# Optimization experiments

Hardware: AMD Instinct MI355X
Metric: run time of the kernel (lower is better)

The kernel has to match this reference:

```python
import jax, jax.numpy as jnp
import numpy as np

N = 8192      # sequence length (rows of query/key/value)
D = 768       # model dim (Conv1d in_channels)
DFF = 2048    # FFN hidden dim (Conv1d out_channels)


def setup_inputs() -> dict:
    key = jax.random.key(0)
    ks = jax.random.split(key, 7)
    query = jax.random.normal(ks[0], (N, D), dtype=jnp.float32)
    k = jax.random.normal(ks[1], (N, D), dtype=jnp.float32)
    value = jax.random.normal(ks[2], (N, D), dtype=jnp.float32)
    # Conv1d(kernel_size=1) == dense layer: weight [out,in], bias [out]
    W1 = jax.random.normal(ks[3], (DFF, D), dtype=jnp.float32) * 0.02
    b1 = jax.random.normal(ks[4], (DFF,), dtype=jnp.float32) * 0.02
    W2 = jax.random.normal(ks[5], (D, DFF), dtype=jnp.float32) * 0.02
    b2 = jax.random.normal(ks[6], (D,), dtype=jnp.float32) * 0.02
    return {"query": query, "key": k, "value": value,
            "W1": W1, "b1": b1, "W2": W2, "b2": b2}


def reference(query, key, value, W1, b1, W2, b2):
    # manual attention: no 1/sqrt(d) scaling in the original module
    scores = jnp.matmul(query, key.T)              # [N, N]
    attn = jax.nn.softmax(scores, axis=-1)         # [N, N]
    context = jnp.matmul(attn, value)              # [N, D]
    # conv1x1 -> ReLU -> conv1x1 (2-layer MLP)
    h = jax.nn.relu(jnp.matmul(context, W1.T) + b1)  # [N, DFF]
    out = jnp.matmul(h, W2.T) + b2                   # [N, D]
    return out
```

## Files before the change

### kernel.cpp

```cpp
#include <hip/hip_runtime.h>
#include <cstdint>
#include <cstddef>

#define DEV __device__ __forceinline__

typedef _Float16 f16;
typedef __attribute__((ext_vector_type(8))) _Float16 f16x8;
typedef __attribute__((ext_vector_type(4))) float f32x4;

DEV unsigned short f2h(float f) {
  f16 h = (f16)f;
  return __builtin_bit_cast(unsigned short, h);
}

DEV void async_ld16(const void* g, void* l) {
  __builtin_amdgcn_global_load_lds(
      (__attribute__((address_space(1))) unsigned int*)(uintptr_t)g,
      (__attribute__((address_space(3))) unsigned int*)(uint32_t)(uintptr_t)l,
      16, 0, 0);
}

#define MFMA16(d, a, b_) (d) = __builtin_amdgcn_mfma_f32_16x16x32_f16((a), (b_), (d), 0, 0, 0)

template <int EPI, bool RELU, bool HASBIAS, bool ALPHA, bool XCD>
__global__ __launch_bounds__(512, 2) void gemm256(
    const unsigned short* __restrict__ A, const unsigned short* __restrict__ B,
    void* __restrict__ Cp, const float* __restrict__ bias,
    const unsigned short* __restrict__ alp, int Mtot,
    int K, int lda, int ldb, int ldc, int nt, int mt, int sl) {
  extern __shared__ char smem[];
  const int NT = K >> 6;

  int mb, nb, zb;
  {
    const int b = blockIdx.x;
    if (XCD) {
      const int xcd = b & 7, q = b >> 3;
      nb = q % nt;
      const int rest = q / nt;
      zb = rest % sl;
      mb = xcd * (mt >> 3) + rest / sl;
    } else {
      nb = b % nt;
      const int t = b / nt;
      mb = t % mt;
      zb = t / mt;
    }
  }
  const int bm = mb << 8, bn = nb << 8;
  const unsigned koff = (unsigned)zb * (unsigned)K;

  const int tid = threadIdx.x;
  const int wave = tid >> 6, lane = tid & 63;
  const int wr = wave >> 2, wc = wave & 3;
  const int mr = lane & 15, quad = lane >> 4;

  const int slot = tid & 7, rr = tid >> 3;
  const int ce = (slot ^ (rr & 7)) << 3;

  f32x4 acc[8][4] = {};
  f16x8 av0[4][2], av1[4][2], bv0[2][2], bv1[2][2];
  const f16* alb = (const f16*)(smem + 131072);

  if (ALPHA) {
    const int ntl = K >> 7;
    const unsigned short* g0 = alp + (size_t)(zb * ntl) * Mtot + bm;
    uint4* s = (uint4*)(smem + 131072);
    const int nu4 = (ntl << 5);
    for (int idx = tid; idx < nu4; idx += 512) {
      const int tt = idx >> 5;
      const int ru = (idx & 31) << 3;
      s[idx] = *(const uint4*)(g0 + (size_t)tt * Mtot + ru);
    }
  }

  auto stA = [&](int h, int Ts) {
    const int t_ = Ts >= NT ? Ts - NT : Ts;
    const unsigned kk = koff + (unsigned)(t_ << 6);
    char* l = smem + ((Ts & 1) << 16) + h * 16384 + wave * 1024;
#pragma unroll
    for (int p = 0; p < 2; ++p) {
      const unsigned off = (unsigned)(bm + p * 128 + h * 64 + rr) * (unsigned)lda + kk + ce;
      async_ld16(A + off, l + p * 8192);
    }
  };
  auto stB = [&](int h, int Ts) {
    const int t_ = Ts >= NT ? Ts - NT : Ts;
    const unsigned kk = koff + (unsigned)(t_ << 6);
    char* l = smem + ((Ts & 1) << 16) + 32768 + h * 16384 + wave * 1024;
#pragma unroll
    for (int p = 0; p < 2; ++p) {
      const unsigned off =
          (unsigned)(bn + p * 128 + (rr >> 5) * 64 + h * 32 + (rr & 31)) * (unsigned)ldb + kk + ce;
      async_ld16(B + off, l + p * 8192);
    }
  };
  auto rdA = [&](int bufc, int i, int ks) {
    const int r = wr * 64 + (i & 3) * 16 + mr;
    return *(const f16x8*)(smem + bufc + (i >> 2) * 16384 + r * 128 +
                           ((((ks << 2) | quad) ^ (mr & 7)) << 4));
  };
  auto rdB = [&](int bufc, int j, int ks) {
    const int r = wc * 32 + (j & 1) * 16 + mr;
    return *(const f16x8*)(smem + bufc + 32768 + (j >> 1) * 16384 + r * 128 +
                           ((((ks << 2) | quad) ^ (mr & 7)) << 4));
  };

  stA(0, 0); stB(0, 0); stA(1, 0); stB(1, 0);
  stA(0, 1); stB(0, 1); stA(1, 1);
  if (ALPHA) asm volatile("s_waitcnt lgkmcnt(0)" ::: "memory");
  asm volatile("s_waitcnt vmcnt(6)" ::: "memory");
  __builtin_amdgcn_s_barrier();

  for (int T = 0; T < NT; ++T) {
    const int bufc = (T & 1) << 16;
    f16 a0_[4], a1_[4];
#pragma unroll
    for (int i = 0; i < 4; ++i) { av0[i][0] = rdA(bufc, i, 0); av0[i][1] = rdA(bufc, i, 1); }
    if (ALPHA) {
#pragma unroll
      for (int i = 0; i < 4; ++i) a0_[i] = alb[(T >> 1) * 256 + wr * 128 + i * 16 + mr];
    }
    stB(1, T + 1);
    __builtin_amdgcn_s_barrier();
    asm volatile("s_waitcnt lgkmcnt(0)" ::: "memory");
    __builtin_amdgcn_sched_barrier(0);
    if (ALPHA) {
#pragma unroll
      for (int i = 0; i < 4; ++i) { av0[i][0] = av0[i][0] * a0_[i]; av0[i][1] = av0[i][1] * a0_[i]; }
    }
    if (T) {
      __builtin_amdgcn_s_setprio(1);
#pragma unroll
      for (int i = 0; i < 4; ++i)
#pragma unroll
        for (int j = 0; j < 2; ++j) {
          MFMA16(acc[4 + i][2 + j], av1[i][0], bv1[j][0]);
          MFMA16(acc[4 + i][2 + j], av1[i][1], bv1[j][1]);
        }
      __builtin_amdgcn_s_setprio(0);
    }
    __builtin_amdgcn_s_barrier();
#pragma unroll
    for (int j = 0; j < 2; ++j) { bv0[j][0] = rdB(bufc, j, 0); bv0[j][1] = rdB(bufc, j, 1); }
    stA(0, T + 2);
    __builtin_amdgcn_s_barrier();
    asm volatile("s_waitcnt lgkmcnt(0)" ::: "memory");
    __builtin_amdgcn_sched_barrier(0);
    __builtin_amdgcn_s_setprio(1);
#pragma unroll
    for (int i = 0; i < 4; ++i)
#pragma unroll
      for (int j = 0; j < 2; ++j) {
        MFMA16(acc[i][j], av0[i][0], bv0[j][0]);
        MFMA16(acc[i][j], av0[i][1], bv0[j][1]);
      }
    __builtin_amdgcn_s_setprio(0);
    __builtin_amdgcn_s_barrier();
#pragma unroll
    for (int i = 0; i < 4; ++i) { av1[i][0] = rdA(bufc, 4 + i, 0); av1[i][1] = rdA(bufc, 4 + i, 1); }
    if (ALPHA) {
#pragma unroll
      for (int i = 0; i < 4; ++i) a1_[i] = alb[(T >> 1) * 256 + wr * 128 + 64 + i * 16 + mr];
    }
    stB(0, T + 2);
    __builtin_amdgcn_s_barrier();
    asm volatile("s_waitcnt lgkmcnt(0)" ::: "memory");
    __builtin_amdgcn_sched_barrier(0);
    if (ALPHA) {
#pragma unroll
      for (int i = 0; i < 4; ++i) { av1[i][0] = av1[i][0] * a1_[i]; av1[i][1] = av1[i][1] * a1_[i]; }
    }
    __builtin_amdgcn_s_setprio(1);
#pragma unroll
    for (int i = 0; i < 4; ++i)
#pragma unroll
      for (int j = 0; j < 2; ++j) {
        MFMA16(acc[4 + i][j], av1[i][0], bv0[j][0]);
        MFMA16(acc[4 + i][j], av1[i][1], bv0[j][1]);
      }
    __builtin_amdgcn_s_setprio(0);
    __builtin_amdgcn_s_barrier();
#pragma unroll
    for (int j = 0; j < 2; ++j) { bv1[j][0] = rdB(bufc, 2 + j, 0); bv1[j][1] = rdB(bufc, 2 + j, 1); }
    stA(1, T + 2);
    __builtin_amdgcn_s_barrier();
    asm volatile("s_waitcnt lgkmcnt(0)" ::: "memory");
    __builtin_amdgcn_sched_barrier(0);
    __builtin_amdgcn_s_setprio(1);
#pragma unroll
    for (int i = 0; i < 4; ++i)
#pragma unroll
      for (int j = 0; j < 2; ++j) {
        MFMA16(acc[i][2 + j], av0[i][0], bv1[j][0]);
        MFMA16(acc[i][2 + j], av0[i][1], bv1[j][1]);
      }
    __builtin_amdgcn_s_setprio(0);
    asm volatile("s_waitcnt vmcnt(6)" ::: "memory");
    __builtin_amdgcn_s_barrier();
  }
  __builtin_amdgcn_s_setprio(1);
#pragma unroll
  for (int i = 0; i < 4; ++i)
#pragma unroll
    for (int j = 0; j < 2; ++j) {
      MFMA16(acc[4 + i][2 + j], av1[i][0], bv1[j][0]);
      MFMA16(acc[4 + i][2 + j], av1[i][1], bv1[j][1]);
    }
  __builtin_amdgcn_s_setprio(0);
  asm volatile("s_waitcnt vmcnt(0)" ::: "memory");
  __builtin_amdgcn_s_barrier();

#pragma unroll
  for (int i = 0; i < 8; ++i) {
#pragma unroll
    for (int j = 0; j < 4; ++j) {
      const int col = bn + wc * 64 + j * 16 + mr;
      float bb = 0.f;
      if (HASBIAS) bb = bias[col];
#pragma unroll
      for (int r = 0; r < 4; ++r) {
        const int row = bm + wr * 128 + i * 16 + quad * 4 + r;
        float v = acc[i][j][r];
        if (HASBIAS) v += bb;
        if (RELU) v = fmaxf(v, 0.f);
        if (EPI == 2)
          atomicAdd(&((float*)Cp)[(size_t)row * ldc + col], v);
        else
          ((unsigned short*)Cp)[(size_t)row * ldc + col] = f2h(v);
      }
    }
  }
}

__global__ __launch_bounds__(512, 2) void qk256(
    const unsigned short* __restrict__ A, const unsigned short* __restrict__ B,
    unsigned short* __restrict__ P, float* __restrict__ stm,
    float* __restrict__ stl, int M, int K, int lda, int ldb, int ldc) {
  extern __shared__ char smem[];
  const int NT = K >> 6;

  const int b = blockIdx.x;
  const int xcd = b & 7, c = b >> 3;
  const int mb = c & 31, nb = (xcd << 2) | (c >> 5);
  const int bm = mb << 8, bn = nb << 8;

  const int tid = threadIdx.x;
  const int wave = tid >> 6, lane = tid & 63;
  const int wr = wave >> 2, wc = wave & 3;
  const int mr = lane & 15, quad = lane >> 4;

  const int slot = tid & 7, rr = tid >> 3;
  const int ce = (slot ^ (rr & 7)) << 3;

  f32x4 acc[8][4] = {};
  f16x8 av0[4][2], av1[4][2], bv0[2][2], bv1[2][2];

  auto stA = [&](int h, int Ts) {
    const int t = Ts >= NT ? Ts - NT : Ts;
    const int kk = t << 6;
    char* l = smem + ((Ts & 1) << 16) + h * 16384 + wave * 1024;
#pragma unroll
    for (int p = 0; p < 2; ++p) {
      const unsigned off = (unsigned)(bm + p * 128 + h * 64 + rr) * (unsigned)lda + kk + ce;
      async_ld16(A + off, l + p * 8192);
    }
  };
  auto stB = [&](int h, int Ts) {
    const int t = Ts >= NT ? Ts - NT : Ts;
    const int kk = t << 6;
    char* l = smem + ((Ts & 1) << 16) + 32768 + h * 16384 + wave * 1024;
#pragma unroll
    for (int p = 0; p < 2; ++p) {
      const unsigned off =
          (unsigned)(bn + p * 128 + (rr >> 5) * 64 + h * 32 + (rr & 31)) * (unsigned)ldb + kk + ce;
      async_ld16(B + off, l + p * 8192);
    }
  };
  auto rdA = [&](int bufc, int i, int ks) {
    const int r = wr * 64 + (i & 3) * 16 + mr;
    return *(const f16x8*)(smem + bufc + (i >> 2) * 16384 + r * 128 +
                           ((((ks << 2) | quad) ^ (mr & 7)) << 4));
  };
  auto rdB = [&](int bufc, int j, int ks) {
    const int r = wc * 32 + (j & 1) * 16 + mr;
    return *(const f16x8*)(smem + bufc + 32768 + (j >> 1) * 16384 + r * 128 +
                           ((((ks << 2) | quad) ^ (mr & 7)) << 4));
  };

  stA(0, 0); stB(0, 0); stA(1, 0); stB(1, 0);
  stA(0, 1); stB(0, 1); stA(1, 1);
  asm volatile("s_waitcnt vmcnt(6)" ::: "memory");
  __builtin_amdgcn_s_barrier();

  for (int T = 0; T < NT; ++T) {
    const int bufc = (T & 1) << 16;
#pragma unroll
    for (int i = 0; i < 4; ++i) { av0[i][0] = rdA(bufc, i, 0); av0[i][1] = rdA(bufc, i, 1); }
    stB(1, T + 1);
    __builtin_amdgcn_s_barrier();
    asm volatile("s_waitcnt lgkmcnt(0)" ::: "memory");
    __builtin_amdgcn_sched_barrier(0);
    if (T) {
      __builtin_amdgcn_s_setprio(1);
#pragma unroll
      for (int i = 0; i < 4; ++i)
#pragma unroll
        for (int j = 0; j < 2; ++j) {
          MFMA16(acc[4 + i][2 + j], av1[i][0], bv1[j][0]);
          MFMA16(acc[4 + i][2 + j], av1[i][1], bv1[j][1]);
        }
      __builtin_amdgcn_s_setprio(0);
    }
    __builtin_amdgcn_s_barrier();
#pragma unroll
    for (int j = 0; j < 2; ++j) { bv0[j][0] = rdB(bufc, j, 0); bv0[j][1] = rdB(bufc, j, 1); }
    stA(0, T + 2);
    __builtin_amdgcn_s_barrier();
    asm volatile("s_waitcnt lgkmcnt(0)" ::: "memory");
    __builtin_amdgcn_sched_barrier(0);
    __builtin_amdgcn_s_setprio(1);
#pragma unroll
    for (int i = 0; i < 4; ++i)
#pragma unroll
      for (int j = 0; j < 2; ++j) {
        MFMA16(acc[i][j], av0[i][0], bv0[j][0]);
        MFMA16(acc[i][j], av0[i][1], bv0[j][1]);
      }
    __builtin_amdgcn_s_setprio(0);
    __builtin_amdgcn_s_barrier();
#pragma unroll
    for (int i = 0; i < 4; ++i) { av1[i][0] = rdA(bufc, 4 + i, 0); av1[i][1] = rdA(bufc, 4 + i, 1); }
    stB(0, T + 2);
    __builtin_amdgcn_s_barrier();
    asm volatile("s_waitcnt lgkmcnt(0)" ::: "memory");
    __builtin_amdgcn_sched_barrier(0);
    __builtin_amdgcn_s_setprio(1);
#pragma unroll
    for (int i = 0; i < 4; ++i)
#pragma unroll
      for (int j = 0; j < 2; ++j) {
        MFMA16(acc[4 + i][j], av1[i][0], bv0[j][0]);
        MFMA16(acc[4 + i][j], av1[i][1], bv0[j][1]);
      }
    __builtin_amdgcn_s_setprio(0);
    __builtin_amdgcn_s_barrier();
#pragma unroll
    for (int j = 0; j < 2; ++j) { bv1[j][0] = rdB(bufc, 2 + j, 0); bv1[j][1] = rdB(bufc, 2 + j, 1); }
    stA(1, T + 2);
    __builtin_amdgcn_s_barrier();
    asm volatile("s_waitcnt lgkmcnt(0)" ::: "memory");
    __builtin_amdgcn_sched_barrier(0);
    __builtin_amdgcn_s_setprio(1);
#pragma unroll
    for (int i = 0; i < 4; ++i)
#pragma unroll
      for (int j = 0; j < 2; ++j) {
        MFMA16(acc[i][2 + j], av0[i][0], bv1[j][0]);
        MFMA16(acc[i][2 + j], av0[i][1], bv1[j][1]);
      }
    __builtin_amdgcn_s_setprio(0);
    asm volatile("s_waitcnt vmcnt(6)" ::: "memory");
    __builtin_amdgcn_s_barrier();
  }
  __builtin_amdgcn_s_setprio(1);
#pragma unroll
  for (int i = 0; i < 4; ++i)
#pragma unroll
    for (int j = 0; j < 2; ++j) {
      MFMA16(acc[4 + i][2 + j], av1[i][0], bv1[j][0]);
      MFMA16(acc[4 + i][2 + j], av1[i][1], bv1[j][1]);
    }
  __builtin_amdgcn_s_setprio(0);
  asm volatile("s_waitcnt vmcnt(0)" ::: "memory");
  __builtin_amdgcn_s_barrier();

  float* sred = (float*)smem;
  float* ssum = (float*)(smem + 4096);
  const int hc = wc >> 1;
  float Mh[8][4];

#pragma unroll
  for (int i = 0; i < 8; ++i)
#pragma unroll
    for (int r = 0; r < 4; ++r) {
      float m = acc[i][0][r];
#pragma unroll
      for (int j = 1; j < 4; ++j) m = fmaxf(m, acc[i][j][r]);
      m = fmaxf(m, __shfl_xor(m, 1));
      m = fmaxf(m, __shfl_xor(m, 2));
      m = fmaxf(m, __shfl_xor(m, 4));
      m = fmaxf(m, __shfl_xor(m, 8));
      if (mr == 0) sred[(wr * 128 + i * 16 + quad * 4 + r) * 4 + wc] = m;
    }
  __syncthreads();
#pragma unroll
  for (int i = 0; i < 8; ++i)
#pragma unroll
    for (int r = 0; r < 4; ++r) {
      const int row_l = wr * 128 + i * 16 + quad * 4 + r;
      Mh[i][r] = fmaxf(sred[row_l * 4 + 2 * hc], sred[row_l * 4 + 2 * hc + 1]);
    }
#pragma unroll
  for (int i = 0; i < 8; ++i)
#pragma unroll
    for (int r = 0; r < 4; ++r) {
      const int row_l = wr * 128 + i * 16 + quad * 4 + r;
      float l = 0.f;
#pragma unroll
      for (int j = 0; j < 4; ++j) {
        const float e = __expf(acc[i][j][r] - Mh[i][r]);
        P[(size_t)(bm + row_l) * ldc + (bn + wc * 64 + j * 16 + mr)] = f2h(e);
        l += e;
      }
      l += __shfl_xor(l, 1);
      l += __shfl_xor(l, 2);
      l += __shfl_xor(l, 4);
      l += __shfl_xor(l, 8);
      if (mr == 0) ssum[row_l * 4 + wc] = l;
    }
  __syncthreads();
  if ((wc & 1) == 0 && mr == 0) {
#pragma unroll
    for (int i = 0; i < 8; ++i)
#pragma unroll
      for (int r = 0; r < 4; ++r) {
        const int row_l = wr * 128 + i * 16 + quad * 4 + r;
        const int tile = nb * 2 + hc;
        stm[(size_t)tile * M + bm + row_l] = Mh[i][r];
        stl[(size_t)tile * M + bm + row_l] =
            ssum[row_l * 4 + 2 * hc] + ssum[row_l * 4 + 2 * hc + 1];
      }
  }
}

__global__ __launch_bounds__(256) void combine_alpha(
    const float* __restrict__ stm, const float* __restrict__ stl,
    unsigned short* __restrict__ alp, int ntile, int Mtot) {
  const int row = blockIdx.x * 4 + (threadIdx.x >> 6);
  const int t = threadIdx.x & 63;
  float m = (t < ntile) ? stm[(size_t)t * Mtot + row] : -1e30f;
  float M = m;
#pragma unroll
  for (int o = 1; o < 64; o <<= 1) M = fmaxf(M, __shfl_xor(M, o));
  float l = (t < ntile) ? stl[(size_t)t * Mtot + row] : 0.f;
  float c = l * __expf(m - M);
#pragma unroll
  for (int o = 1; o < 64; o <<= 1) c += __shfl_xor(c, o);
  if (t < ntile) alp[(size_t)t * Mtot + row] = f2h(__expf(m - M) / c);
}

__global__ __launch_bounds__(256) void cvt_f16(const float* __restrict__ in,
                                               unsigned short* __restrict__ out, int n) {
  int i = blockIdx.x * 256 + threadIdx.x;
  if (i < n) out[i] = f2h(in[i]);
}

__global__ __launch_bounds__(256) void bias_fill(float* __restrict__ out,
                                                 const float* __restrict__ b, int d) {
  int i = blockIdx.x * 256 + threadIdx.x;
  out[i] = b[i % d];
}

__global__ __launch_bounds__(256) void vt_kernel(const float* __restrict__ V,
                                                 unsigned short* __restrict__ vT) {
  __shared__ float t[32][33];
  const int bx = blockIdx.x, by = blockIdx.y;
  const int x = threadIdx.x, y = threadIdx.y;
#pragma unroll
  for (int r = 0; r < 4; ++r)
    t[y + r * 8][x] = V[(size_t)(by * 32 + y + r * 8) * 768 + bx * 32 + x];
  __syncthreads();
#pragma unroll
  for (int r = 0; r < 4; ++r)
    vT[(size_t)(bx * 32 + y + r * 8) * 8192 + by * 32 + x] = f2h(t[x][y + r * 8]);
}

extern "C" void kernel_launch(void* const* d_in, const int* in_sizes, int n_in,
                              void* d_out, int out_size, void* d_ws, size_t ws_size,
                              hipStream_t stream) {
  const int N = 8192, D = 768, DFF = 2048;
  const float* Q  = (const float*)d_in[0];
  const float* Km = (const float*)d_in[1];
  const float* V  = (const float*)d_in[2];
  const float* W1 = (const float*)d_in[3];
  const float* b1 = (const float*)d_in[4];
  const float* W2 = (const float*)d_in[5];
  const float* b2 = (const float*)d_in[6];

  char* w = (char*)d_ws;
  size_t off = 0;
  auto take = [&](size_t bytes) { void* p = w + off; off += bytes; return p; };
  unsigned short* qh   = (unsigned short*)take((size_t)N * D * 2);
  unsigned short* kh   = (unsigned short*)take((size_t)N * D * 2);
  unsigned short* vT   = (unsigned short*)take((size_t)N * D * 2);
  unsigned short* ctx16= (unsigned short*)take((size_t)N * D * 2);
  float*          ctx32= (float*)take((size_t)N * D * 4);
  unsigned short* hb   = (unsigned short*)take((size_t)N * DFF * 2);
  unsigned short* w1h  = (unsigned short*)take((size_t)DFF * D * 2);
  unsigned short* w2h  = (unsigned short*)take((size_t)D * DFF * 2);
  float*          stm  = (float*)take((size_t)64 * N * 4);
  float*          stl  = (float*)take((size_t)64 * N * 4);
  unsigned short* alp  = (unsigned short*)take((size_t)64 * N * 2);
  unsigned short* Pp   = (unsigned short*)take((size_t)N * N * 2);
  (void)ws_size;

  cvt_f16<<<(N * D) / 256, 256, 0, stream>>>(Q, qh, N * D);
  cvt_f16<<<(N * D) / 256, 256, 0, stream>>>(Km, kh, N * D);
  vt_kernel<<<dim3(D / 32, N / 32), dim3(32, 8), 0, stream>>>(V, vT);
  cvt_f16<<<(DFF * D) / 256, 256, 0, stream>>>(W1, w1h, DFF * D);
  cvt_f16<<<(D * DFF) / 256, 256, 0, stream>>>(W2, w2h, D * DFF);
  hipMemsetAsync(ctx32, 0, (size_t)N * D * 4, stream);
  bias_fill<<<(N * D) / 256, 256, 0, stream>>>((float*)d_out, b2, D);

  {
    hipFuncSetAttribute((const void*)qk256,
                        hipFuncAttributeMaxDynamicSharedMemorySize, 131072);
    qk256<<<(N / 256) * (N / 256), 512, 131072, stream>>>(
        qh, kh, Pp, stm, stl, N, D, D, D, N);
  }
  combine_alpha<<<N / 4, 256, 0, stream>>>(stm, stl, alp, 64, N);

  {
    const int nt = D / 256, mt = N / 256, sl = 2;
    const int smem_sz = 131072 + ((N / sl) >> 7) * 256 * 2;
    hipFuncSetAttribute((const void*)gemm256<2, false, false, true, true>,
                        hipFuncAttributeMaxDynamicSharedMemorySize, smem_sz);
    gemm256<2, false, false, true, true><<<nt * mt * sl, 512, smem_sz, stream>>>(
        Pp, vT, ctx32, nullptr, alp, N,
        N / sl, N, N, D, nt, mt, sl);
  }
  cvt_f16<<<(N * D) / 256, 256, 0, stream>>>(ctx32, ctx16, N * D);

  {
    const int nt = DFF / 256, mt = N / 256;
    hipFuncSetAttribute((const void*)gemm256<0, true, true, false, true>,
                        hipFuncAttributeMaxDynamicSharedMemorySize, 131072);
    gemm256<0, true, true, false, true><<<nt * mt, 512, 131072, stream>>>(
        ctx16, w1h, hb, b1, nullptr, N,
        D, D, D, DFF, nt, mt, 1);
  }
  {
    const int nt = D / 256, mt = N / 256, sl = 2;
    hipFuncSetAttribute((const void*)gemm256<2, false, false, false, true>,
                        hipFuncAttributeMaxDynamicSharedMemorySize, 131072);
    gemm256<2, false, false, false, true><<<nt * mt * sl, 512, 131072, stream>>>(
        hb, w2h, (float*)d_out, nullptr, nullptr, N,
        DFF / sl, DFF, DFF, D, nt, mt, sl);
  }
}
```

Baseline: 576.0 us.

## Add 256x192 tile variant for D-output GEMMs to improve CU fill

Templates the GEMM on output tile width BN and adds a 192-column variant with its own B-tile LDS layout, load mapping and fragment reads. The attention-times-V and second FFN GEMMs (output width 768) now use 256x192 tiles, so 4 N-tiles instead of 3 and more workgroups to fill the GPU. The trade-offs are lower arithmetic intensity per tile, an uneven LDS load split for the B operand, and more atomic split-K traffic in total.

```diff
diff --git a/kernel.cpp b/kernel.cpp
--- a/kernel.cpp
+++ b/kernel.cpp
@@ -22,13 +22,16 @@
 
 #define MFMA16(d, a, b_) (d) = __builtin_amdgcn_mfma_f32_16x16x32_f16((a), (b_), (d), 0, 0, 0)
 
-template <int EPI, bool RELU, bool HASBIAS, bool ALPHA, bool XCD>
+template <int BN, int EPI, bool RELU, bool HASBIAS, bool ALPHA, bool XCD>
 __global__ __launch_bounds__(512, 2) void gemm256(
     const unsigned short* __restrict__ A, const unsigned short* __restrict__ B,
     void* __restrict__ Cp, const float* __restrict__ bias,
     const unsigned short* __restrict__ alp, int Mtot,
     int K, int lda, int ldb, int ldc, int nt, int mt, int sl) {
   extern __shared__ char smem[];
+  constexpr int FN = BN / 64;
+  constexpr int WCW = BN / 4;
+  constexpr int BUFSZ = 32768 + BN * 128;
   const int NT = K >> 6;
 
   int mb, nb, zb;
@@ -47,7 +50,7 @@
       zb = t / mt;
     }
   }
-  const int bm = mb << 8, bn = nb << 8;
+  const int bm = mb << 8, bn = nb * BN;
   const unsigned koff = (unsigned)zb * (unsigned)K;
 
   const int tid = threadIdx.x;
@@ -58,14 +61,14 @@
   const int slot = tid & 7, rr = tid >> 3;
   const int ce = (slot ^ (rr & 7)) << 3;
 
-  f32x4 acc[8][4] = {};
-  f16x8 av0[4][2], av1[4][2], bv0[2][2], bv1[2][2];
-  const f16* alb = (const f16*)(smem + 131072);
+  f32x4 acc[8][FN] = {};
+  f16x8 av0[4][2], av1[4][2], bv0[2][2], bv1[FN - 2][2];
+  const f16* alb = (const f16*)(smem + 2 * BUFSZ);
 
   if (ALPHA) {
     const int ntl = K >> 7;
     const unsigned short* g0 = alp + (size_t)(zb * ntl) * Mtot + bm;
-    uint4* s = (uint4*)(smem + 131072);
+    uint4* s = (uint4*)(smem + 2 * BUFSZ);
     const int nu4 = (ntl << 5);
     for (int idx = tid; idx < nu4; idx += 512) {
       const int tt = idx >> 5;
@@ -77,7 +80,7 @@
   auto stA = [&](int h, int Ts) {
     const int t_ = Ts >= NT ? Ts - NT : Ts;
     const unsigned kk = koff + (unsigned)(t_ << 6);
-    char* l = smem + ((Ts & 1) << 16) + h * 16384 + wave * 1024;
+    char* l = smem + (Ts & 1) * BUFSZ + h * 16384 + wave * 1024;
 #pragma unroll
     for (int p = 0; p < 2; ++p) {
       const unsigned off = (unsigned)(bm + p * 128 + h * 64 + rr) * (unsigned)lda + kk + ce;
@@ -87,12 +90,22 @@
   auto stB = [&](int h, int Ts) {
     const int t_ = Ts >= NT ? Ts - NT : Ts;
     const unsigned kk = koff + (unsigned)(t_ << 6);
-    char* l = smem + ((Ts & 1) << 16) + 32768 + h * 16384 + wave * 1024;
-#pragma unroll
-    for (int p = 0; p < 2; ++p) {
-      const unsigned off =
-          (unsigned)(bn + p * 128 + (rr >> 5) * 64 + h * 32 + (rr & 31)) * (unsigned)ldb + kk + ce;
-      async_ld16(B + off, l + p * 8192);
+    char* l = smem + (Ts & 1) * BUFSZ + 32768 + h * 16384 + wave * 1024;
+    if (BN == 256) {
+#pragma unroll
+      for (int p = 0; p < 2; ++p) {
+        const int g = bn + p * 128 + (rr >> 5) * 64 + h * 32 + (rr & 31);
+        async_ld16(B + ((unsigned)g * (unsigned)ldb + kk + ce), l + p * 8192);
+      }
+    } else if (h == 0) {
+#pragma unroll
+      for (int p = 0; p < 2; ++p) {
+        const int g = bn + (p * 2 + (rr >> 5)) * 48 + (rr & 31);
+        async_ld16(B + ((unsigned)g * (unsigned)ldb + kk + ce), l + p * 8192);
+      }
+    } else {
+      const int g = bn + (rr >> 4) * 48 + 32 + (rr & 15);
+      async_ld16(B + ((unsigned)g * (unsigned)ldb + kk + ce), l);
     }
   };
   auto rdA = [&](int bufc, int i, int ks) {
@@ -100,9 +113,14 @@
     return *(const f16x8*)(smem + bufc + (i >> 2) * 16384 + r * 128 +
                            ((((ks << 2) | quad) ^ (mr & 7)) << 4));
   };
-  auto rdB = [&](int bufc, int j, int ks) {
-    const int r = wc * 32 + (j & 1) * 16 + mr;
-    return *(const f16x8*)(smem + bufc + 32768 + (j >> 1) * 16384 + r * 128 +
+  auto rdB0 = [&](int bufc, int j, int ks) {
+    const int rb = wc * 32 + j * 16 + mr;
+    return *(const f16x8*)(smem + bufc + 32768 + rb * 128 +
+                           ((((ks << 2) | quad) ^ (mr & 7)) << 4));
+  };
+  auto rdB1 = [&](int bufc, int j, int ks) {
+    const int rb = (BN == 256) ? (wc * 32 + (j - 2) * 16 + mr) : (wc * 16 + mr);
+    return *(const f16x8*)(smem + bufc + 32768 + 16384 + rb * 128 +
                            ((((ks << 2) | quad) ^ (mr & 7)) << 4));
   };
 
@@ -113,7 +131,7 @@
   __builtin_amdgcn_s_barrier();
 
   for (int T = 0; T < NT; ++T) {
-    const int bufc = (T & 1) << 16;
+    const int bufc = (T & 1) * BUFSZ;
     f16 a0_[4], a1_[4];
 #pragma unroll
     for (int i = 0; i < 4; ++i) { av0[i][0] = rdA(bufc, i, 0); av0[i][1] = rdA(bufc, i, 1); }
@@ -134,7 +152,7 @@
 #pragma unroll
       for (int i = 0; i < 4; ++i)
 #pragma unroll
-        for (int j = 0; j < 2; ++j) {
+        for (int j = 0; j < FN - 2; ++j) {
           MFMA16(acc[4 + i][2 + j], av1[i][0], bv1[j][0]);
           MFMA16(acc[4 + i][2 + j], av1[i][1], bv1[j][1]);
         }
@@ -142,7 +160,7 @@
     }
     __builtin_amdgcn_s_barrier();
 #pragma unroll
-    for (int j = 0; j < 2; ++j) { bv0[j][0] = rdB(bufc, j, 0); bv0[j][1] = rdB(bufc, j, 1); }
+    for (int j = 0; j < 2; ++j) { bv0[j][0] = rdB0(bufc, j, 0); bv0[j][1] = rdB0(bufc, j, 1); }
     stA(0, T + 2);
     __builtin_amdgcn_s_barrier();
     asm volatile("s_waitcnt lgkmcnt(0)" ::: "memory");
@@ -182,7 +200,7 @@
     __builtin_amdgcn_s_setprio(0);
     __builtin_amdgcn_s_barrier();
 #pragma unroll
-    for (int j = 0; j < 2; ++j) { bv1[j][0] = rdB(bufc, 2 + j, 0); bv1[j][1] = rdB(bufc, 2 + j, 1); }
+    for (int j = 0; j < FN - 2; ++j) { bv1[j][0] = rdB1(bufc, 2 + j, 0); bv1[j][1] = rdB1(bufc, 2 + j, 1); }
     stA(1, T + 2);
     __builtin_amdgcn_s_barrier();
     asm volatile("s_waitcnt lgkmcnt(0)" ::: "memory");
@@ -191,7 +209,7 @@
 #pragma unroll
     for (int i = 0; i < 4; ++i)
 #pragma unroll
-      for (int j = 0; j < 2; ++j) {
+      for (int j = 0; j < FN - 2; ++j) {
         MFMA16(acc[i][2 + j], av0[i][0], bv1[j][0]);
         MFMA16(acc[i][2 + j], av0[i][1], bv1[j][1]);
       }
@@ -203,7 +221,7 @@
 #pragma unroll
   for (int i = 0; i < 4; ++i)
 #pragma unroll
-    for (int j = 0; j < 2; ++j) {
+    for (int j = 0; j < FN - 2; ++j) {
       MFMA16(acc[4 + i][2 + j], av1[i][0], bv1[j][0]);
       MFMA16(acc[4 + i][2 + j], av1[i][1], bv1[j][1]);
     }
@@ -214,8 +232,8 @@
 #pragma unroll
   for (int i = 0; i < 8; ++i) {
 #pragma unroll
-    for (int j = 0; j < 4; ++j) {
-      const int col = bn + wc * 64 + j * 16 + mr;
+    for (int j = 0; j < FN; ++j) {
+      const int col = bn + wc * WCW + j * 16 + mr;
       float bb = 0.f;
       if (HASBIAS) bb = bias[col];
 #pragma unroll
@@ -522,11 +540,12 @@
   combine_alpha<<<N / 4, 256, 0, stream>>>(stm, stl, alp, 64, N);
 
   {
-    const int nt = D / 256, mt = N / 256, sl = 2;
-    const int smem_sz = 131072 + ((N / sl) >> 7) * 256 * 2;
-    hipFuncSetAttribute((const void*)gemm256<2, false, false, true, true>,
+    const int nt = D / 192, mt = N / 256, sl = 2;
+    constexpr int BUFSZ = 32768 + 192 * 128;
+    const int smem_sz = 2 * BUFSZ + ((N / 2) >> 7) * 256 * 2;
+    hipFuncSetAttribute((const void*)gemm256<192, 2, false, false, true, true>,
                         hipFuncAttributeMaxDynamicSharedMemorySize, smem_sz);
-    gemm256<2, false, false, true, true><<<nt * mt * sl, 512, smem_sz, stream>>>(
+    gemm256<192, 2, false, false, true, true><<<nt * mt * sl, 512, smem_sz, stream>>>(
         Pp, vT, ctx32, nullptr, alp, N,
         N / sl, N, N, D, nt, mt, sl);
   }
@@ -534,17 +553,18 @@
 
   {
     const int nt = DFF / 256, mt = N / 256;
-    hipFuncSetAttribute((const void*)gemm256<0, true, true, false, true>,
+    hipFuncSetAttribute((const void*)gemm256<256, 0, true, true, false, true>,
                         hipFuncAttributeMaxDynamicSharedMemorySize, 131072);
-    gemm256<0, true, true, false, true><<<nt * mt, 512, 131072, stream>>>(
+    gemm256<256, 0, true, true, false, true><<<nt * mt, 512, 131072, stream>>>(
         ctx16, w1h, hb, b1, nullptr, N,
         D, D, D, DFF, nt, mt, 1);
   }
   {
-    const int nt = D / 256, mt = N / 256, sl = 2;
-    hipFuncSetAttribute((const void*)gemm256<2, false, false, false, true>,
-                        hipFuncAttributeMaxDynamicSharedMemorySize, 131072);
-    gemm256<2, false, false, false, true><<<nt * mt * sl, 512, 131072, stream>>>(
+    const int nt = D / 192, mt = N / 256, sl = 2;
+    constexpr int BUFSZ = 32768 + 192 * 128;
+    hipFuncSetAttribute((const void*)gemm256<192, 2, false, false, false, true>,
+                        hipFuncAttributeMaxDynamicSharedMemorySize, 2 * BUFSZ);
+    gemm256<192, 2, false, false, false, true><<<nt * mt * sl, 512, 2 * BUFSZ, stream>>>(
         hb, w2h, (float*)d_out, nullptr, nullptr, N,
         DFF / sl, DFF, DFF, D, nt, mt, sl);
   }
```

Result: faster. 553.3 us (-4.0%).
